# Kernel tuning notes

Hardware: AMD Instinct MI355X
Metric: run time of the kernel (lower is better)

## Reference

```python
import jax, jax.numpy as jnp
import numpy as np

HIDDEN = 32  # channel dim; rfft -> 17 complex bins

def setup_inputs() -> dict:
    key = jax.random.key(0)
    ks = jax.random.split(key, 5)
    x = jax.random.normal(ks[0], (64, 8192, HIDDEN), dtype=jnp.float32)
    half = HIDDEN // 2 + 1  # 17
    # parameters initialized like torch.randn * 0.02
    cm1_real = jax.random.normal(ks[1], (1, 1, half), dtype=jnp.float32) * 0.02
    cm1_imag = jax.random.normal(ks[2], (1, 1, half), dtype=jnp.float32) * 0.02
    cm2_real = jax.random.normal(ks[3], (1, 1, half), dtype=jnp.float32) * 0.02
    cm2_imag = jax.random.normal(ks[4], (1, 1, half), dtype=jnp.float32) * 0.02
    return {"x": x, "cm1_real": cm1_real, "cm1_imag": cm1_imag,
            "cm2_real": cm2_real, "cm2_imag": cm2_imag}

def reference(x, cm1_real, cm1_imag, cm2_real, cm2_imag):
    # complex mixing weights (nn.Parameter(torch.complex(real, imag)))
    cm1 = jax.lax.complex(cm1_real, cm1_imag)  # [1,1,17]
    cm2 = jax.lax.complex(cm2_real, cm2_imag)  # [1,1,17]
    # DFT_ along channel dim (orthonormal real FFT)
    xf = jnp.fft.rfft(x, axis=-1, norm="ortho")            # [B,F,17] complex64
    # Sine nonlinearity (w0=1) on complex values, sandwiched by complex gates
    xf = jnp.sin(xf * cm1) * cm2
    # IDFT_ back to length HIDDEN channels
    return jnp.fft.irfft(xf, n=HIDDEN, axis=-1, norm="ortho")  # [B,F,32] float32
```

## Files before the change

### kernel.cpp

```cpp
#include <hip/hip_runtime.h>
#include <math.h>

#define NCH 32
#define TPB 256

constexpr float CT[32] = {
   1.0f,                 0.9807852804032304f,  0.9238795325112867f,  0.8314696123025452f,
   0.7071067811865476f,  0.5555702330196022f,  0.3826834323650898f,  0.1950903220161283f,
   0.0f,                -0.1950903220161283f, -0.3826834323650898f, -0.5555702330196022f,
  -0.7071067811865476f, -0.8314696123025452f, -0.9238795325112867f, -0.9807852804032304f,
  -1.0f,                -0.9807852804032304f, -0.9238795325112867f, -0.8314696123025452f,
  -0.7071067811865476f, -0.5555702330196022f, -0.3826834323650898f, -0.1950903220161283f,
   0.0f,                 0.1950903220161283f,  0.3826834323650898f,  0.5555702330196022f,
   0.7071067811865476f,  0.8314696123025452f,  0.9238795325112867f,  0.9807852804032304f
};
constexpr float ST[32] = {
   0.0f,                 0.1950903220161283f,  0.3826834323650898f,  0.5555702330196022f,
   0.7071067811865476f,  0.8314696123025452f,  0.9238795325112867f,  0.9807852804032304f,
   1.0f,                 0.9807852804032304f,  0.9238795325112867f,  0.8314696123025452f,
   0.7071067811865476f,  0.5555702330196022f,  0.3826834323650898f,  0.1950903220161283f,
   0.0f,                -0.1950903220161283f, -0.3826834323650898f, -0.5555702330196022f,
  -0.7071067811865476f, -0.8314696123025452f, -0.9238795325112867f, -0.9807852804032304f,
  -1.0f,                -0.9807852804032304f, -0.9238795325112867f, -0.8314696123025452f,
  -0.7071067811865476f, -0.5555702330196022f, -0.3826834323650898f, -0.1950903220161283f
};

__device__ __forceinline__ void cnonlin(float sr, float si,
    float w1r, float w1i, float w2r, float w2i, float& G, float& H)
{
    const float p = fmaf(sr, w1r, si * w1i);
    const float q = fmaf(sr, w1i, -(si * w1r));
    float sp, cp;
    __sincosf(p, &sp, &cp);
    const float eq = __expf(q), en = __expf(-q);
    const float sA = sp * (eq + en);
    const float sB = cp * (eq - en);
    G = fmaf(sA, w2r, -(sB * w2i));
    H = fmaf(sA, w2i, sB * w2r);
}

__device__ __forceinline__ float cnonlin_real(float sr,
    float w1r, float w1i, float w2r, float w2i)
{
    const float p = sr * w1r;
    const float q = sr * w1i;
    float sp, cp;
    __sincosf(p, &sp, &cp);
    const float eq = __expf(q), en = __expf(-q);
    return fmaf(sp * (eq + en), w2r, -((cp * (eq - en)) * w2i));
}

__global__ __launch_bounds__(TPB, 4) void fcm_kernel(
    const float* __restrict__ x,
    const float* __restrict__ c1r, const float* __restrict__ c1i,
    const float* __restrict__ c2r, const float* __restrict__ c2i,
    float* __restrict__ out)
{
    const long long row = (long long)blockIdx.x * TPB + threadIdx.x;
    const float* xp_ptr = x + row * NCH;
    float*       op_ptr = out + row * NCH;
    const float inv = 0.17677669529663687f;

    float xr[NCH];
    #pragma unroll
    for (int i = 0; i < 8; ++i) {
        float4 v = *reinterpret_cast<const float4*>(xp_ptr + i * 4);
        xr[i * 4 + 0] = v.x; xr[i * 4 + 1] = v.y;
        xr[i * 4 + 2] = v.z; xr[i * 4 + 3] = v.w;
    }

    float ev[16], od[16];
    #pragma unroll
    for (int m = 1; m <= 15; ++m) {
        ev[m] = xr[m] + xr[32 - m];
        od[m] = xr[m] - xr[32 - m];
    }
    const float xp = xr[0] + xr[16], xm = xr[0] - xr[16];
    const float e8 = ev[8], o8 = od[8];
    float ep[8], em[8], opp[8], om[8];
    #pragma unroll
    for (int m = 1; m <= 7; ++m) {
        ep[m]  = ev[m] + ev[16 - m];
        em[m]  = ev[m] - ev[16 - m];
        opp[m] = od[m] + od[16 - m];
        om[m]  = od[m] - od[16 - m];
    }

    float Gp[8], Gm[8], Hp[8], Hm[8];
    float G0, G16, G8, H8;

    {
        const float A  = ep[2] + ep[4] + ep[6];
        const float B  = ep[1] + ep[3] + ep[5] + ep[7];
        const float b0 = xp + e8;
        const float sr0  = b0 + A + B;
        const float sr16 = b0 + A - B;
        G0  = cnonlin_real(sr0,  c1r[0]  * inv, c1i[0]  * inv,
                           c2r[0]  * (0.5f * inv), c2i[0]  * (0.5f * inv));
        G16 = cnonlin_real(sr16, c1r[16] * inv, c1i[16] * inv,
                           c2r[16] * (0.5f * inv), c2i[16] * (0.5f * inv));
        const float sr8 = b0 - ep[2] + ep[4] - ep[6];
        const float si8 = om[1] - om[3] + om[5] - om[7];
        cnonlin(sr8, si8, c1r[8] * inv, c1i[8] * inv,
                c2r[8] * inv, c2i[8] * inv, G8, H8);
    }

    #pragma unroll
    for (int k = 1; k <= 7; ++k) {
        const int kp = 16 - k;
        const bool kodd = (k & 1);
        const float u1 = kodd ? em[1] : ep[1],  u3 = kodd ? em[3] : ep[3];
        const float u5 = kodd ? em[5] : ep[5],  u7 = kodd ? em[7] : ep[7];
        const float u2 = kodd ? em[2] : ep[2],  u4 = kodd ? em[4] : ep[4];
        const float u6 = kodd ? em[6] : ep[6];
        const float v1 = kodd ? opp[1] : om[1], v3 = kodd ? opp[3] : om[3];
        const float v5 = kodd ? opp[5] : om[5], v7 = kodd ? opp[7] : om[7];
        const float v2 = kodd ? opp[2] : om[2], v4 = kodd ? opp[4] : om[4];
        const float v6 = kodd ? opp[6] : om[6];

        const float SrE = fmaf(CT[(2*k)&31], u2, fmaf(CT[(4*k)&31], u4, CT[(6*k)&31] * u6));
        const float SrO = fmaf(CT[k&31], u1, fmaf(CT[(3*k)&31], u3,
                          fmaf(CT[(5*k)&31], u5, CT[(7*k)&31] * u7)));
        const float SiE = fmaf(ST[(2*k)&31], v2, fmaf(ST[(4*k)&31], v4, ST[(6*k)&31] * v6));
        const float SiO = fmaf(ST[k&31], v1, fmaf(ST[(3*k)&31], v3,
                          fmaf(ST[(5*k)&31], v5, ST[(7*k)&31] * v7)));

        const float tb = kodd ? xm : (xp + (((k & 2) == 0) ? e8 : -e8));
        float SiEO  = SiE + SiO;
        float SiOmE = SiO - SiE;
        if (kodd) {
            const float s8 = ((k & 2) == 0) ? o8 : -o8;
            SiEO  += s8;
            SiOmE -= s8;
        }
        const float srk  = tb + SrE + SrO;
        const float srkp = tb + (SrE - SrO);

        float Gk, Hk, Gkp, Hkp;
        cnonlin(srk,  SiEO,  c1r[k]  * inv, c1i[k]  * inv,
                c2r[k]  * inv, c2i[k]  * inv, Gk,  Hk);
        cnonlin(srkp, SiOmE, c1r[kp] * inv, c1i[kp] * inv,
                c2r[kp] * inv, c2i[kp] * inv, Gkp, Hkp);
        Gp[k] = Gk + Gkp;  Gm[k] = Gk - Gkp;
        Hp[k] = Hk + Hkp;  Hm[k] = Hk - Hkp;
    }

    float y[NCH];
    const float Dp = G0 + G16, Dm = G0 - G16;

    {
        const float GA = Gp[2] + Gp[4] + Gp[6];
        const float GB = Gp[1] + Gp[3] + Gp[5] + Gp[7];
        const float b8 = Dp + G8;
        y[0]  = b8 + GA + GB;
        y[16] = b8 + GA - GB;
        const float C8 = -Gp[2] + Gp[4] - Gp[6];
        const float S8 =  Hm[1] - Hm[3] + Hm[5] - Hm[7];
        const float t8 = b8 + C8;
        y[8]  = t8 - S8;
        y[24] = t8 + S8;
    }

    #pragma unroll
    for (int n = 1; n <= 7; ++n) {
        const bool nodd = (n & 1);
        const float g1 = nodd ? Gm[1] : Gp[1], g3 = nodd ? Gm[3] : Gp[3];
        const float g5 = nodd ? Gm[5] : Gp[5], g7 = nodd ? Gm[7] : Gp[7];
        const float g2 = nodd ? Gm[2] : Gp[2], g4 = nodd ? Gm[4] : Gp[4];
        const float g6 = nodd ? Gm[6] : Gp[6];
        const float h1 = nodd ? Hp[1] : Hm[1], h3 = nodd ? Hp[3] : Hm[3];
        const float h5 = nodd ? Hp[5] : Hm[5], h7 = nodd ? Hp[7] : Hm[7];
        const float h2 = nodd ? Hp[2] : Hm[2], h4 = nodd ? Hp[4] : Hm[4];
        const float h6 = nodd ? Hp[6] : Hm[6];

        const float CE = fmaf(CT[(2*n)&31], g2, fmaf(CT[(4*n)&31], g4, CT[(6*n)&31] * g6));
        const float CO = fmaf(CT[n&31], g1, fmaf(CT[(3*n)&31], g3,
                         fmaf(CT[(5*n)&31], g5, CT[(7*n)&31] * g7)));
        const float SE = fmaf(ST[(2*n)&31], h2, fmaf(ST[(4*n)&31], h4, ST[(6*n)&31] * h6));
        const float SO = fmaf(ST[n&31], h1, fmaf(ST[(3*n)&31], h3,
                         fmaf(ST[(5*n)&31], h5, ST[(7*n)&31] * h7)));

        const float a = CE + CO, b = CE - CO, c = SE + SO, d = SE - SO;
        float w1, w2;
        if (nodd) {
            const float P = ((n & 2) == 0) ? H8 : -H8;
            w1 = Dm - P;  w2 = Dm + P;
        } else {
            w1 = Dp + (((n & 2) == 0) ? G8 : -G8);
            w2 = w1;
        }
        y[n]      = w1 + a - c;
        y[32 - n] = w2 + a + c;
        y[16 - n] = w2 + b + d;
        y[16 + n] = w1 + b - d;
    }

    #pragma unroll
    for (int i = 0; i < 8; ++i) {
        float4 v;
        v.x = y[i * 4 + 0]; v.y = y[i * 4 + 1];
        v.z = y[i * 4 + 2]; v.w = y[i * 4 + 3];
        *reinterpret_cast<float4*>(op_ptr + i * 4) = v;
    }
}

extern "C" void kernel_launch(void* const* d_in, const int* in_sizes, int n_in,
                              void* d_out, int out_size, void* d_ws, size_t ws_size,
                              hipStream_t stream) {
    const float* x   = (const float*)d_in[0];
    const float* c1r = (const float*)d_in[1];
    const float* c1i = (const float*)d_in[2];
    const float* c2r = (const float*)d_in[3];
    const float* c2i = (const float*)d_in[4];
    float* out = (float*)d_out;

    const int total  = in_sizes[0];
    const int blocks = total / (TPB * NCH);
    fcm_kernel<<<blocks, TPB, 0, stream>>>(x, c1r, c1i, c2r, c2i, out);
}
```

Measured before the change: 130.3 us.

## Process four rows per thread with double-buffered register prefetch

Result: no change. 131.8 us (+1.2%).

```diff
diff --git a/kernel.cpp b/kernel.cpp
--- a/kernel.cpp
+++ b/kernel.cpp
@@ -3,6 +3,7 @@
 
 #define NCH 32
 #define TPB 256
+#define ROWS 4
 
 constexpr float CT[32] = {
    1.0f,                 0.9807852804032304f,  0.9238795325112867f,  0.8314696123025452f,
@@ -50,24 +51,12 @@
     return fmaf(sp * (eq + en), w2r, -((cp * (eq - en)) * w2i));
 }
 
-__global__ __launch_bounds__(TPB, 4) void fcm_kernel(
-    const float* __restrict__ x,
+__device__ __forceinline__ void process_row(
+    const float* __restrict__ xr, float* __restrict__ y,
     const float* __restrict__ c1r, const float* __restrict__ c1i,
-    const float* __restrict__ c2r, const float* __restrict__ c2i,
-    float* __restrict__ out)
-{
-    const long long row = (long long)blockIdx.x * TPB + threadIdx.x;
-    const float* xp_ptr = x + row * NCH;
-    float*       op_ptr = out + row * NCH;
+    const float* __restrict__ c2r, const float* __restrict__ c2i)
+{
     const float inv = 0.17677669529663687f;
-
-    float xr[NCH];
-    #pragma unroll
-    for (int i = 0; i < 8; ++i) {
-        float4 v = *reinterpret_cast<const float4*>(xp_ptr + i * 4);
-        xr[i * 4 + 0] = v.x; xr[i * 4 + 1] = v.y;
-        xr[i * 4 + 2] = v.z; xr[i * 4 + 3] = v.w;
-    }
 
     float ev[16], od[16];
     #pragma unroll
@@ -88,21 +77,18 @@
 
     float Gp[8], Gm[8], Hp[8], Hm[8];
     float G0, G16, G8, H8;
-
     {
         const float A  = ep[2] + ep[4] + ep[6];
         const float B  = ep[1] + ep[3] + ep[5] + ep[7];
         const float b0 = xp + e8;
-        const float sr0  = b0 + A + B;
-        const float sr16 = b0 + A - B;
-        G0  = cnonlin_real(sr0,  c1r[0]  * inv, c1i[0]  * inv,
-                           c2r[0]  * (0.5f * inv), c2i[0]  * (0.5f * inv));
-        G16 = cnonlin_real(sr16, c1r[16] * inv, c1i[16] * inv,
-                           c2r[16] * (0.5f * inv), c2i[16] * (0.5f * inv));
+        G0  = cnonlin_real(b0 + A + B,  c1r[0]*inv,  c1i[0]*inv,
+                           c2r[0]*(0.5f*inv),  c2i[0]*(0.5f*inv));
+        G16 = cnonlin_real(b0 + A - B,  c1r[16]*inv, c1i[16]*inv,
+                           c2r[16]*(0.5f*inv), c2i[16]*(0.5f*inv));
         const float sr8 = b0 - ep[2] + ep[4] - ep[6];
         const float si8 = om[1] - om[3] + om[5] - om[7];
-        cnonlin(sr8, si8, c1r[8] * inv, c1i[8] * inv,
-                c2r[8] * inv, c2i[8] * inv, G8, H8);
+        cnonlin(sr8, si8, c1r[8]*inv, c1i[8]*inv, c2r[8]*inv, c2i[8]*inv,
+                G8, H8);
     }
 
     #pragma unroll
@@ -137,17 +123,15 @@
         const float srkp = tb + (SrE - SrO);
 
         float Gk, Hk, Gkp, Hkp;
-        cnonlin(srk,  SiEO,  c1r[k]  * inv, c1i[k]  * inv,
-                c2r[k]  * inv, c2i[k]  * inv, Gk,  Hk);
-        cnonlin(srkp, SiOmE, c1r[kp] * inv, c1i[kp] * inv,
-                c2r[kp] * inv, c2i[kp] * inv, Gkp, Hkp);
+        cnonlin(srk,  SiEO,  c1r[k]*inv,  c1i[k]*inv,  c2r[k]*inv,  c2i[k]*inv,
+                Gk, Hk);
+        cnonlin(srkp, SiOmE, c1r[kp]*inv, c1i[kp]*inv, c2r[kp]*inv, c2i[kp]*inv,
+                Gkp, Hkp);
         Gp[k] = Gk + Gkp;  Gm[k] = Gk - Gkp;
         Hp[k] = Hk + Hkp;  Hm[k] = Hk - Hkp;
     }
 
-    float y[NCH];
     const float Dp = G0 + G16, Dm = G0 - G16;
-
     {
         const float GA = Gp[2] + Gp[4] + Gp[6];
         const float GB = Gp[1] + Gp[3] + Gp[5] + Gp[7];
@@ -194,14 +178,45 @@
         y[16 - n] = w2 + b + d;
         y[16 + n] = w1 + b - d;
     }
-
-    #pragma unroll
-    for (int i = 0; i < 8; ++i) {
-        float4 v;
-        v.x = y[i * 4 + 0]; v.y = y[i * 4 + 1];
-        v.z = y[i * 4 + 2]; v.w = y[i * 4 + 3];
-        *reinterpret_cast<float4*>(op_ptr + i * 4) = v;
-    }
+}
+
+#define LOADROW(DST, I) do {                                                   \
+    const float* p_ = x + ((long long)blockIdx.x * (TPB * ROWS)                \
+                           + (I) * TPB + threadIdx.x) * NCH;                   \
+    _Pragma("unroll")                                                          \
+    for (int j_ = 0; j_ < 8; ++j_) {                                           \
+        float4 v_ = *reinterpret_cast<const float4*>(p_ + j_ * 4);             \
+        DST[j_*4+0] = v_.x; DST[j_*4+1] = v_.y;                                \
+        DST[j_*4+2] = v_.z; DST[j_*4+3] = v_.w;                                \
+    }                                                                          \
+} while (0)
+
+#define STOREROW(SRC, I) do {                                                  \
+    float* p_ = out + ((long long)blockIdx.x * (TPB * ROWS)                    \
+                       + (I) * TPB + threadIdx.x) * NCH;                       \
+    _Pragma("unroll")                                                          \
+    for (int j_ = 0; j_ < 8; ++j_) {                                           \
+        *reinterpret_cast<float4*>(p_ + j_ * 4) =                              \
+            make_float4(SRC[j_*4+0], SRC[j_*4+1], SRC[j_*4+2], SRC[j_*4+3]);   \
+    }                                                                          \
+} while (0)
+
+__global__ __launch_bounds__(TPB) void fcm_kernel(
+    const float* __restrict__ x,
+    const float* __restrict__ c1r, const float* __restrict__ c1i,
+    const float* __restrict__ c2r, const float* __restrict__ c2i,
+    float* __restrict__ out)
+{
+    float xa[NCH], xb[NCH], y[NCH];
+
+    LOADROW(xa, 0);
+    LOADROW(xb, 1);
+    process_row(xa, y, c1r, c1i, c2r, c2i);  STOREROW(y, 0);
+    LOADROW(xa, 2);
+    process_row(xb, y, c1r, c1i, c2r, c2i);  STOREROW(y, 1);
+    LOADROW(xb, 3);
+    process_row(xa, y, c1r, c1i, c2r, c2i);  STOREROW(y, 2);
+    process_row(xb, y, c1r, c1i, c2r, c2i);  STOREROW(y, 3);
 }
 
 extern "C" void kernel_launch(void* const* d_in, const int* in_sizes, int n_in,
@@ -215,6 +230,6 @@
     float* out = (float*)d_out;
 
     const int total  = in_sizes[0];
-    const int blocks = total / (TPB * NCH);
+    const int blocks = total / (TPB * ROWS * NCH);
     fcm_kernel<<<blocks, TPB, 0, stream>>>(x, c1r, c1i, c2r, c2i, out);
 }
```
